# Performance work log

Measured on AMD Instinct MI355X. Metric: run time of the kernel, lower is better.

The kernel has to match this reference:

```python
import jax, jax.numpy as jnp
import numpy as np

EPS = 1e-5

def _bn_relu(y, mean, var, scale, bias):
    # y: (b, c, n); eval-mode batchnorm over channel axis, then ReLU
    inv = scale / jnp.sqrt(var + EPS)
    return jax.nn.relu((y - mean[None, :, None]) * inv[None, :, None] + bias[None, :, None])

def setup_inputs() -> dict:
    key = jax.random.key(0)
    ks = jax.random.split(key, 6)
    b, c, n, cr = 4, 256, 4096, 32
    inp = {
        'x': jax.random.normal(ks[0], (b, c, n), jnp.float32),
        'w_q': jax.random.normal(ks[1], (cr, c), jnp.float32) * (1.0 / np.sqrt(c)),
        'w_k': jax.random.normal(ks[2], (cr, c), jnp.float32) * (1.0 / np.sqrt(c)),
        'w_v': jax.random.normal(ks[3], (c, c), jnp.float32) * (1.0 / np.sqrt(c)),
        'bn1_scale': jnp.ones((cr,), jnp.float32), 'bn1_bias': jnp.zeros((cr,), jnp.float32),
        'bn1_mean': jnp.zeros((cr,), jnp.float32), 'bn1_var': jnp.ones((cr,), jnp.float32),
        'bn2_scale': jnp.ones((cr,), jnp.float32), 'bn2_bias': jnp.zeros((cr,), jnp.float32),
        'bn2_mean': jnp.zeros((cr,), jnp.float32), 'bn2_var': jnp.ones((cr,), jnp.float32),
        'bn3_scale': jnp.ones((c,), jnp.float32), 'bn3_bias': jnp.zeros((c,), jnp.float32),
        'bn3_mean': jnp.zeros((c,), jnp.float32), 'bn3_var': jnp.ones((c,), jnp.float32),
        'gamma': jax.random.normal(ks[4], (1,), jnp.float32),
    }
    return inp

def reference(x, w_q, w_k, w_v,
              bn1_scale, bn1_bias, bn1_mean, bn1_var,
              bn2_scale, bn2_bias, bn2_mean, bn2_var,
              bn3_scale, bn3_bias, bn3_mean, bn3_var,
              gamma):
    # x: (b, c, n). Original views as (b, c, n, 1) so width=1, height=n.
    b, c, n = x.shape
    # 1x1 conv == channel matmul, then BN+ReLU
    q = _bn_relu(jnp.einsum('oc,bcn->bon', w_q, x), bn1_mean, bn1_var, bn1_scale, bn1_bias)  # (b, c', n)
    k = _bn_relu(jnp.einsum('oc,bcn->bon', w_k, x), bn2_mean, bn2_var, bn2_scale, bn2_bias)  # (b, c', n)
    v = _bn_relu(jnp.einsum('oc,bcn->bon', w_v, x), bn3_mean, bn3_var, bn3_scale, bn3_bias)  # (b, c, n)
    # energy_H: (b, n, n) with -inf diagonal (self-attention along 'height')
    energy_h = jnp.einsum('bdi,bdj->bij', q, k)
    eye = jnp.eye(n, dtype=bool)
    energy_h = jnp.where(eye[None], -jnp.inf, energy_h)
    # energy_W: width=1 -> per-position self energy (b, n)
    energy_w = jnp.sum(q * k, axis=1)
    # softmax over concat of n H-logits and 1 W-logit
    att = jax.nn.softmax(jnp.concatenate([energy_h, energy_w[..., None]], axis=-1), axis=-1)  # (b, n, n+1)
    att_h = att[..., :n]        # (b, n, n), query i -> key j
    att_w = att[..., n]         # (b, n)
    out_h = jnp.einsum('bcj,bij->bci', v, att_h)   # aggregate values along height
    out_w = v * att_w[:, None, :]                  # width=1 self term
    out = gamma[0] * (out_h + out_w) + x
    return out
```

## Files before the change

kernel.cpp:

```cpp
#include <hip/hip_runtime.h>

#define Bb 4
#define Cc 256
#define Nn 4096
#define CR 32
#define EPS_BN 1e-5f
#define SHIFT2 28.853900817779268f
#define LOG2E  1.4426950408889634f
#define JSPLIT 4
#define JSL (Nn / JSPLIT)
#define TJ 64
#define NTILES (JSL / TJ)

typedef __attribute__((ext_vector_type(8))) short short8;
typedef __attribute__((ext_vector_type(4))) float f32x4;

__device__ inline unsigned int pk2(float a, float b) {
    __bf16 ha = (__bf16)a, hb = (__bf16)b;
    unsigned short ra = __builtin_bit_cast(unsigned short, ha);
    unsigned short rb = __builtin_bit_cast(unsigned short, hb);
    return ((unsigned int)rb << 16) | ra;
}
__device__ inline float blo(unsigned int u) { return __uint_as_float(u << 16); }
__device__ inline float bhi(unsigned int u) { return __uint_as_float(u & 0xffff0000u); }
__device__ inline float ex2(float x) { return __builtin_amdgcn_exp2f(x); }

__global__ __launch_bounds__(256) void qkv_kernel(
    const float* __restrict__ x,
    const float* __restrict__ wq, const float* __restrict__ wk, const float* __restrict__ wv,
    const float* __restrict__ bn1s, const float* __restrict__ bn1b, const float* __restrict__ bn1m, const float* __restrict__ bn1v,
    const float* __restrict__ bn2s, const float* __restrict__ bn2b, const float* __restrict__ bn2m, const float* __restrict__ bn2v,
    const float* __restrict__ bn3s, const float* __restrict__ bn3b, const float* __restrict__ bn3m, const float* __restrict__ bn3v,
    __bf16* __restrict__ Qt, __bf16* __restrict__ Kt, __bf16* __restrict__ Vb)
{
    __shared__ __align__(16) __bf16 F[16384];
    __shared__ __align__(16) float  sXf[4][32 * 40];
    __shared__ __align__(16) __bf16 sXt[4][2][32 * 40];

    const int tid = threadIdx.x;
    const int n0 = blockIdx.x * 128, g = blockIdx.y, b = blockIdx.z;
    const int lane = tid & 63, w = tid >> 6;
    const int l15 = lane & 15, l4 = lane >> 4;

    {
        int r = tid >> 2, q = tid & 3;
        int R = g * 64 + r;
        const float* src = (R < 32) ? (wq + (size_t)R * Cc)
                         : (R < 64) ? (wk + (size_t)(R - 32) * Cc)
                                    : (wv + (size_t)(R - 64) * Cc);
        int mt = r >> 4, l15r = r & 15;
#pragma unroll
        for (int u8 = 0; u8 < 8; ++u8) {
            float4 a = *(const float4*)&src[q * 64 + u8 * 8];
            float4 c2 = *(const float4*)&src[q * 64 + u8 * 8 + 4];
            uint4 p = { pk2(a.x,a.y), pk2(a.z,a.w), pk2(c2.x,c2.y), pk2(c2.z,c2.w) };
            int kc = 2 * q + (u8 >> 2), l4k = u8 & 3;
            *(uint4*)&F[(((kc * 4 + mt) * 64 + l4k * 16 + l15r)) * 8] = p;
        }
    }

    float*  sXfw  = &sXf[w][0];
    __bf16* sXtw0 = &sXt[w][0][0];
    __bf16* sXtw1 = &sXt[w][1][0];

    const int cr = lane >> 3, nq = lane & 7;
    const float* xbase = x + (size_t)(b * Cc + cr) * Nn + n0 + w * 32 + nq * 4;

    float4 xg[4];
#pragma unroll
    for (int it = 0; it < 4; ++it)
        xg[it] = *(const float4*)&xbase[(size_t)(it * 8) * Nn];

    __syncthreads();

    f32x4 acc[4][2];
#pragma unroll
    for (int mt = 0; mt < 4; ++mt)
#pragma unroll
        for (int nt = 0; nt < 2; ++nt) acc[mt][nt] = (f32x4){0.f, 0.f, 0.f, 0.f};

    for (int kc = 0; kc < 8; ++kc) {
#pragma unroll
        for (int it = 0; it < 4; ++it)
            *(float4*)&sXfw[(it * 8 + cr) * 40 + nq * 4] = xg[it];

        if (kc + 1 < 8) {
#pragma unroll
            for (int it = 0; it < 4; ++it)
                xg[it] = *(const float4*)&xbase[(size_t)((kc + 1) * 32 + it * 8) * Nn];
        }

#pragma unroll
        for (int s = 0; s < 2; ++s) {
            int n = lane & 31, c0 = (lane >> 5) * 8 + s * 16;
            float h[8], lo[8];
#pragma unroll
            for (int j = 0; j < 8; ++j) {
                float v = sXfw[(c0 + j) * 40 + n];
                float hh = (float)(__bf16)v;
                h[j] = hh; lo[j] = v - hh;
            }
            uint4 H = { pk2(h[0],h[1]), pk2(h[2],h[3]), pk2(h[4],h[5]), pk2(h[6],h[7]) };
            uint4 L = { pk2(lo[0],lo[1]), pk2(lo[2],lo[3]), pk2(lo[4],lo[5]), pk2(lo[6],lo[7]) };
            *(uint4*)&sXtw0[n * 40 + c0] = H;
            *(uint4*)&sXtw1[n * 40 + c0] = L;
        }

        short8 bh[2], bl[2];
#pragma unroll
        for (int nt = 0; nt < 2; ++nt) {
            bh[nt] = *(const short8*)&sXtw0[(nt * 16 + l15) * 40 + l4 * 8];
            bl[nt] = *(const short8*)&sXtw1[(nt * 16 + l15) * 40 + l4 * 8];
        }
#pragma unroll
        for (int mt = 0; mt < 4; ++mt) {
            short8 af = *(const short8*)&F[((kc * 4 + mt) * 64 + lane) * 8];
#pragma unroll
            for (int nt = 0; nt < 2; ++nt) {
                acc[mt][nt] = __builtin_amdgcn_mfma_f32_16x16x32_bf16(af, bh[nt], acc[mt][nt], 0, 0, 0);
                acc[mt][nt] = __builtin_amdgcn_mfma_f32_16x16x32_bf16(af, bl[nt], acc[mt][nt], 0, 0, 0);
            }
        }
    }

    if (g == 0) {
#pragma unroll
        for (int mt = 0; mt < 4; ++mt) {
            float scl[4], off[4];
#pragma unroll
            for (int r = 0; r < 4; ++r) {
                int R = mt * 16 + l4 * 4 + r;
                float s, o;
                if (R < 32) {
                    s = bn1s[R] * __frsqrt_rn(bn1v[R] + EPS_BN);
                    o = bn1b[R] - bn1m[R] * s;
                } else {
                    int row = R - 32;
                    s = bn2s[row] * __frsqrt_rn(bn2v[row] + EPS_BN);
                    o = bn2b[row] - bn2m[row] * s;
                    s *= LOG2E; o *= LOG2E;
                }
                scl[r] = s; off[r] = o;
            }
            __bf16* dst = (mt < 2) ? Qt : Kt;
            int d0 = (mt & 1) * 16 + l4 * 4;
#pragma unroll
            for (int nt = 0; nt < 2; ++nt) {
                f32x4 a = acc[mt][nt];
                float e0 = fmaxf(fmaf(a.x, scl[0], off[0]), 0.f);
                float e1 = fmaxf(fmaf(a.y, scl[1], off[1]), 0.f);
                float e2 = fmaxf(fmaf(a.z, scl[2], off[2]), 0.f);
                float e3 = fmaxf(fmaf(a.w, scl[3], off[3]), 0.f);
                uint2 p = { pk2(e0, e1), pk2(e2, e3) };
                int n = n0 + w * 32 + nt * 16 + l15;
                *(uint2*)&dst[(size_t)(b * Nn + n) * CR + d0] = p;
            }
        }
    } else {
        __bf16* oT = F;
        __syncthreads();
#pragma unroll
        for (int mt = 0; mt < 4; ++mt) {
            float scl[4], off[4];
#pragma unroll
            for (int r = 0; r < 4; ++r) {
                int row = (g - 1) * 64 + mt * 16 + l4 * 4 + r;
                float s = bn3s[row] * __frsqrt_rn(bn3v[row] + EPS_BN);
                scl[r] = s; off[r] = bn3b[row] - bn3m[row] * s;
            }
#pragma unroll
            for (int nt = 0; nt < 2; ++nt) {
                f32x4 a = acc[mt][nt];
                float e[4];
                e[0] = fmaxf(fmaf(a.x, scl[0], off[0]), 0.f);
                e[1] = fmaxf(fmaf(a.y, scl[1], off[1]), 0.f);
                e[2] = fmaxf(fmaf(a.z, scl[2], off[2]), 0.f);
                e[3] = fmaxf(fmaf(a.w, scl[3], off[3]), 0.f);
                int ncol = w * 32 + nt * 16 + l15;
#pragma unroll
                for (int r = 0; r < 4; ++r)
                    oT[(mt * 16 + l4 * 4 + r) * 136 + ncol] = (__bf16)e[r];
            }
        }
        __syncthreads();
        int rr = tid >> 2, qq = tid & 3;
        size_t vrow = (size_t)(b * Cc + (g - 1) * 64 + rr) * Nn + n0 + qq * 32;
#pragma unroll
        for (int e8 = 0; e8 < 4; ++e8)
            *(uint4*)&Vb[vrow + e8 * 8] = *(const uint4*)&oT[rr * 136 + qq * 32 + e8 * 8];
    }
}

__global__ __launch_bounds__(256) void attn_kernel(
    const __bf16* __restrict__ Qt, const __bf16* __restrict__ Kt,
    const __bf16* __restrict__ Vb,
    __bf16* __restrict__ PO, float* __restrict__ PL)
{
    __shared__ __align__(16) __bf16 sQ[64 * 40];
    __shared__ __align__(16) __bf16 sP[64 * 72];
    __shared__ __align__(16) float  sL[4][64];

    const int tid = threadIdx.x, lane = tid & 63, w = tid >> 6;
    const int b = blockIdx.z, js = blockIdx.y, iblk = blockIdx.x;
    const int i0 = iblk * 64;
    const int l15 = lane & 15, l4 = lane >> 4;

    {
        int i = tid >> 2, o = tid & 3;
        *(uint4*)&sQ[i * 40 + o * 8] =
            *(const uint4*)&Qt[(size_t)(b * Nn + i0 + i) * CR + o * 8];
    }
    __syncthreads();
    short8 qf[4];
#pragma unroll
    for (int it = 0; it < 4; ++it)
        qf[it] = *(const short8*)&sQ[(it * 16 + l15) * 40 + l4 * 8];

    f32x4 oacc[16];
#pragma unroll
    for (int z = 0; z < 16; ++z) oacc[z] = (f32x4){0.f, 0.f, 0.f, 0.f};
    float lp[4] = {0.f, 0.f, 0.f, 0.f};

    const size_t jb = (size_t)js * JSL;
    short8 kf = *(const short8*)&Kt[(size_t)(b * Nn + jb + 16 * w + l15) * CR + l4 * 8];

    for (int t = 0; t < NTILES; ++t) {
        const size_t j0 = jb + (size_t)t * TJ;

        short8 vf[8];
#pragma unroll
        for (int u = 0; u < 8; ++u) {
            int jh = u >> 2, ct = u & 3;
            int c = w * 64 + ct * 16 + l15;
            vf[u] = *(const short8*)&Vb[(size_t)(b * Cc + c) * Nn + j0 + (jh * 4 + l4) * 8];
        }

#pragma unroll
        for (int it = 0; it < 4; ++it) {
            f32x4 c0 = (f32x4){0.f, 0.f, 0.f, 0.f};
            c0 = __builtin_amdgcn_mfma_f32_16x16x32_bf16(kf, qf[it], c0, 0, 0, 0);
            float e0 = ex2(c0.x - SHIFT2);
            float e1 = ex2(c0.y - SHIFT2);
            float e2 = ex2(c0.z - SHIFT2);
            float e3 = ex2(c0.w - SHIFT2);
            lp[it] += (e0 + e1) + (e2 + e3);
            uint2 p2 = { pk2(e0, e1), pk2(e2, e3) };
            *(uint2*)&sP[(it * 16 + l15) * 72 + w * 16 + l4 * 4] = p2;
        }
        __syncthreads();

        if (t + 1 < NTILES)
            kf = *(const short8*)&Kt[(size_t)(b * Nn + j0 + TJ + 16 * w + l15) * CR + l4 * 8];

#pragma unroll
        for (int jh = 0; jh < 2; ++jh) {
            short8 pf[4];
#pragma unroll
            for (int it = 0; it < 4; ++it)
                pf[it] = *(const short8*)&sP[(it * 16 + l15) * 72 + jh * 32 + l4 * 8];
#pragma unroll
            for (int ct = 0; ct < 4; ++ct) {
#pragma unroll
                for (int it = 0; it < 4; ++it)
                    oacc[it * 4 + ct] = __builtin_amdgcn_mfma_f32_16x16x32_bf16(
                        pf[it], vf[jh * 4 + ct], oacc[it * 4 + ct], 0, 0, 0);
            }
        }
        __syncthreads();
    }

#pragma unroll
    for (int it = 0; it < 4; ++it) {
        float v = lp[it];
        v += __shfl_xor(v, 16);
        v += __shfl_xor(v, 32);
        if (lane < 16) sL[w][it * 16 + lane] = v;
    }
    __syncthreads();
    if (tid < 64)
        PL[(size_t)(js * Bb + b) * Nn + i0 + tid] =
            sL[0][tid] + sL[1][tid] + sL[2][tid] + sL[3][tid];

    const size_t base = (size_t)((js * Bb + b) * (Nn / 64) + iblk) * 16384;
#pragma unroll
    for (int it = 0; it < 4; ++it)
#pragma unroll
        for (int ct = 0; ct < 4; ++ct) {
            f32x4 a = oacc[it * 4 + ct];
            uint2 p = { pk2(a.x, a.y), pk2(a.z, a.w) };
            *(uint2*)&PO[base + (size_t)((((w * 4 + it) * 4 + ct) * 64 + lane)) * 4] = p;
        }
}

__global__ __launch_bounds__(256) void reduce_kernel(
    const __bf16* __restrict__ PO, const float* __restrict__ PL,
    const float* __restrict__ x, const float* __restrict__ gamma,
    float* __restrict__ out)
{
    __shared__ __align__(16) float oT[64 * 68];
    __shared__ float sLinv[64];

    const int tid = threadIdx.x;
    const int iblk = blockIdx.x, wq = blockIdx.y, b = blockIdx.z;
    const int i0 = iblk * 64;
    const int lane = tid & 63, ct = tid >> 6, l15 = lane & 15, l4 = lane >> 4;

    if (tid < 64) {
        float l = 0.f;
#pragma unroll
        for (int js = 0; js < JSPLIT; ++js)
            l += PL[(size_t)(js * Bb + b) * Nn + i0 + tid];
        sLinv[tid] = 1.0f / l;
    }

    float o[4][4];
#pragma unroll
    for (int it = 0; it < 4; ++it) {
        o[it][0] = o[it][1] = o[it][2] = o[it][3] = 0.f;
#pragma unroll
        for (int js = 0; js < JSPLIT; ++js) {
            size_t base = (size_t)((js * Bb + b) * (Nn / 64) + iblk) * 16384;
            uint2 v = *(const uint2*)&PO[base + (size_t)((((wq * 4 + it) * 4 + ct) * 64 + lane)) * 4];
            o[it][0] += blo(v.x); o[it][1] += bhi(v.x);
            o[it][2] += blo(v.y); o[it][3] += bhi(v.y);
        }
    }

    const int cl = ct * 16 + l15;
#pragma unroll
    for (int it = 0; it < 4; ++it) {
        float4 t4 = { o[it][0], o[it][1], o[it][2], o[it][3] };
        *(float4*)&oT[cl * 68 + it * 16 + l4 * 4] = t4;
    }
    __syncthreads();

    const float g = gamma[0];
    const int c_l = tid >> 2, icol = (tid & 3) * 16;
    const int cg = wq * 64 + c_l;
    const size_t gb = (size_t)(b * Cc + cg) * Nn + i0 + icol;
#pragma unroll
    for (int k4 = 0; k4 < 4; ++k4) {
        float4 ov = *(const float4*)&oT[c_l * 68 + icol + k4 * 4];
        float4 li = *(const float4*)&sLinv[icol + k4 * 4];
        float4 xv = *(const float4*)&x[gb + k4 * 4];
        float4 res;
        res.x = fmaf(g, ov.x * li.x, xv.x);
        res.y = fmaf(g, ov.y * li.y, xv.y);
        res.z = fmaf(g, ov.z * li.z, xv.z);
        res.w = fmaf(g, ov.w * li.w, xv.w);
        *(float4*)&out[gb + k4 * 4] = res;
    }
}

extern "C" void kernel_launch(void* const* d_in, const int* in_sizes, int n_in,
                              void* d_out, int out_size, void* d_ws, size_t ws_size,
                              hipStream_t stream)
{
    const float* x    = (const float*)d_in[0];
    const float* wq   = (const float*)d_in[1];
    const float* wk   = (const float*)d_in[2];
    const float* wv   = (const float*)d_in[3];
    const float* bn1s = (const float*)d_in[4];
    const float* bn1b = (const float*)d_in[5];
    const float* bn1m = (const float*)d_in[6];
    const float* bn1v = (const float*)d_in[7];
    const float* bn2s = (const float*)d_in[8];
    const float* bn2b = (const float*)d_in[9];
    const float* bn2m = (const float*)d_in[10];
    const float* bn2v = (const float*)d_in[11];
    const float* bn3s = (const float*)d_in[12];
    const float* bn3b = (const float*)d_in[13];
    const float* bn3m = (const float*)d_in[14];
    const float* bn3v = (const float*)d_in[15];
    const float* gmm  = (const float*)d_in[16];
    float* out = (float*)d_out;

    char* ws = (char*)d_ws;
    __bf16* Qt  = (__bf16*)(ws);
    __bf16* Kt  = (__bf16*)(ws + (1u << 20));
    __bf16* Vb  = (__bf16*)(ws + (2u << 20));
    char*   big = ws + (10u << 20);
    __bf16* PO  = (__bf16*)big;
    float*  PL  = (float*)(big + 33554432);

    qkv_kernel<<<dim3(Nn / 128, 5, Bb), 256, 0, stream>>>(
        x, wq, wk, wv,
        bn1s, bn1b, bn1m, bn1v,
        bn2s, bn2b, bn2m, bn2v,
        bn3s, bn3b, bn3m, bn3v,
        Qt, Kt, Vb);

    attn_kernel<<<dim3(Nn / 64, JSPLIT, Bb), 256, 0, stream>>>(Qt, Kt, Vb, PO, PL);

    reduce_kernel<<<dim3(Nn / 64, 4, Bb), 256, 0, stream>>>(PO, PL, x, gmm, out);
}
```

Before: 214.6 us.

## Give each wave a private 32x128 attention tile and drop block barriers

The attention kernel now splits the 64-query by 256-channel output so each wave owns 32 queries and 128 channels. Each wave computes its own P tile redundantly and stores it in wave-private, XOR-swizzled shared memory, which removes all __syncthreads in the inner loop and the shared staging of Q and the partial sums. V loads are split into two halves interleaved with the score computation. The trade-off is that the QK^T MFMAs and exponentials are duplicated across the two channel halves. The PO layout and the reduce kernel's indexing change to match.

```diff
diff --git a/kernel.cpp b/kernel.cpp
--- a/kernel.cpp
+++ b/kernel.cpp
@@ -196,99 +196,126 @@
     const __bf16* __restrict__ Vb,
     __bf16* __restrict__ PO, float* __restrict__ PL)
 {
-    __shared__ __align__(16) __bf16 sQ[64 * 40];
-    __shared__ __align__(16) __bf16 sP[64 * 72];
-    __shared__ __align__(16) float  sL[4][64];
+    __shared__ __align__(16) __bf16 sP[4][32 * 64];
 
     const int tid = threadIdx.x, lane = tid & 63, w = tid >> 6;
+    const int wi = w >> 1, wc = w & 1;
     const int b = blockIdx.z, js = blockIdx.y, iblk = blockIdx.x;
     const int i0 = iblk * 64;
-    const int l15 = lane & 15, l4 = lane >> 4;
-
-    {
-        int i = tid >> 2, o = tid & 3;
-        *(uint4*)&sQ[i * 40 + o * 8] =
-            *(const uint4*)&Qt[(size_t)(b * Nn + i0 + i) * CR + o * 8];
-    }
-    __syncthreads();
-    short8 qf[4];
-#pragma unroll
-    for (int it = 0; it < 4; ++it)
-        qf[it] = *(const short8*)&sQ[(it * 16 + l15) * 40 + l4 * 8];
-
-    f32x4 oacc[16];
-#pragma unroll
-    for (int z = 0; z < 16; ++z) oacc[z] = (f32x4){0.f, 0.f, 0.f, 0.f};
-    float lp[4] = {0.f, 0.f, 0.f, 0.f};
+    const int q = lane & 15, h = lane >> 4, q7 = lane & 7;
+
+    char* sPw = (char*)&sP[w][0];
+
+    short8 qf[2];
+#pragma unroll
+    for (int it = 0; it < 2; ++it)
+        qf[it] = *(const short8*)&Qt[(size_t)(b * Nn + i0 + wi * 32 + it * 16 + q) * CR + h * 8];
+
+    f32x4 oacc[2][8];
+#pragma unroll
+    for (int it = 0; it < 2; ++it)
+#pragma unroll
+        for (int ct = 0; ct < 8; ++ct) oacc[it][ct] = (f32x4){0.f, 0.f, 0.f, 0.f};
+    float lp[2] = {0.f, 0.f};
 
     const size_t jb = (size_t)js * JSL;
-    short8 kf = *(const short8*)&Kt[(size_t)(b * Nn + jb + 16 * w + l15) * CR + l4 * 8];
+
+    short8 kf[4];
+#pragma unroll
+    for (int s = 0; s < 4; ++s)
+        kf[s] = *(const short8*)&Kt[(size_t)(b * Nn + jb + s * 16 + q) * CR + h * 8];
+
+    const __bf16* vbase = Vb + (size_t)(b * Cc + wc * 128 + q) * Nn;
 
     for (int t = 0; t < NTILES; ++t) {
         const size_t j0 = jb + (size_t)t * TJ;
 
         short8 vf[8];
 #pragma unroll
-        for (int u = 0; u < 8; ++u) {
-            int jh = u >> 2, ct = u & 3;
-            int c = w * 64 + ct * 16 + l15;
-            vf[u] = *(const short8*)&Vb[(size_t)(b * Cc + c) * Nn + j0 + (jh * 4 + l4) * 8];
-        }
-
-#pragma unroll
-        for (int it = 0; it < 4; ++it) {
-            f32x4 c0 = (f32x4){0.f, 0.f, 0.f, 0.f};
-            c0 = __builtin_amdgcn_mfma_f32_16x16x32_bf16(kf, qf[it], c0, 0, 0, 0);
-            float e0 = ex2(c0.x - SHIFT2);
-            float e1 = ex2(c0.y - SHIFT2);
-            float e2 = ex2(c0.z - SHIFT2);
-            float e3 = ex2(c0.w - SHIFT2);
-            lp[it] += (e0 + e1) + (e2 + e3);
-            uint2 p2 = { pk2(e0, e1), pk2(e2, e3) };
-            *(uint2*)&sP[(it * 16 + l15) * 72 + w * 16 + l4 * 4] = p2;
-        }
-        __syncthreads();
-
-        if (t + 1 < NTILES)
-            kf = *(const short8*)&Kt[(size_t)(b * Nn + j0 + TJ + 16 * w + l15) * CR + l4 * 8];
-
-#pragma unroll
-        for (int jh = 0; jh < 2; ++jh) {
-            short8 pf[4];
-#pragma unroll
-            for (int it = 0; it < 4; ++it)
-                pf[it] = *(const short8*)&sP[(it * 16 + l15) * 72 + jh * 32 + l4 * 8];
-#pragma unroll
-            for (int ct = 0; ct < 4; ++ct) {
-#pragma unroll
-                for (int it = 0; it < 4; ++it)
-                    oacc[it * 4 + ct] = __builtin_amdgcn_mfma_f32_16x16x32_bf16(
-                        pf[it], vf[jh * 4 + ct], oacc[it * 4 + ct], 0, 0, 0);
-            }
-        }
-        __syncthreads();
-    }
-
-#pragma unroll
-    for (int it = 0; it < 4; ++it) {
+        for (int ct = 0; ct < 8; ++ct)
+            vf[ct] = *(const short8*)&vbase[(size_t)(ct * 16) * Nn + j0 + h * 8];
+
+#pragma unroll
+        for (int jss = 0; jss < 2; ++jss) {
+#pragma unroll
+            for (int it = 0; it < 2; ++it) {
+                f32x4 c0 = (f32x4){0.f, 0.f, 0.f, 0.f};
+                c0 = __builtin_amdgcn_mfma_f32_16x16x32_bf16(kf[jss], qf[it], c0, 0, 0, 0);
+                float e0 = ex2(c0.x - SHIFT2), e1 = ex2(c0.y - SHIFT2);
+                float e2 = ex2(c0.z - SHIFT2), e3 = ex2(c0.w - SHIFT2);
+                lp[it] += (e0 + e1) + (e2 + e3);
+                uint2 p2 = { pk2(e0, e1), pk2(e2, e3) };
+                *(uint2*)(sPw + ((it * 16 + q) << 7) + ((((jss << 1) + (h >> 1)) ^ q7) << 4) + ((h & 1) << 3)) = p2;
+            }
+        }
+
+        {
+            short8 pa[2];
+#pragma unroll
+            for (int it = 0; it < 2; ++it)
+                pa[it] = *(const short8*)(sPw + ((it * 16 + q) << 7) + ((h ^ q7) << 4));
+#pragma unroll
+            for (int ct = 0; ct < 8; ++ct) {
+                oacc[0][ct] = __builtin_amdgcn_mfma_f32_16x16x32_bf16(pa[0], vf[ct], oacc[0][ct], 0, 0, 0);
+                oacc[1][ct] = __builtin_amdgcn_mfma_f32_16x16x32_bf16(pa[1], vf[ct], oacc[1][ct], 0, 0, 0);
+            }
+        }
+
+#pragma unroll
+        for (int ct = 0; ct < 8; ++ct)
+            vf[ct] = *(const short8*)&vbase[(size_t)(ct * 16) * Nn + j0 + 32 + h * 8];
+
+#pragma unroll
+        for (int jss = 2; jss < 4; ++jss) {
+#pragma unroll
+            for (int it = 0; it < 2; ++it) {
+                f32x4 c0 = (f32x4){0.f, 0.f, 0.f, 0.f};
+                c0 = __builtin_amdgcn_mfma_f32_16x16x32_bf16(kf[jss], qf[it], c0, 0, 0, 0);
+                float e0 = ex2(c0.x - SHIFT2), e1 = ex2(c0.y - SHIFT2);
+                float e2 = ex2(c0.z - SHIFT2), e3 = ex2(c0.w - SHIFT2);
+                lp[it] += (e0 + e1) + (e2 + e3);
+                uint2 p2 = { pk2(e0, e1), pk2(e2, e3) };
+                *(uint2*)(sPw + ((it * 16 + q) << 7) + ((((jss << 1) + (h >> 1)) ^ q7) << 4) + ((h & 1) << 3)) = p2;
+            }
+        }
+
+        if (t + 1 < NTILES) {
+#pragma unroll
+            for (int s = 0; s < 4; ++s)
+                kf[s] = *(const short8*)&Kt[(size_t)(b * Nn + j0 + TJ + s * 16 + q) * CR + h * 8];
+        }
+
+        {
+            short8 pa[2];
+#pragma unroll
+            for (int it = 0; it < 2; ++it)
+                pa[it] = *(const short8*)(sPw + ((it * 16 + q) << 7) + (((4 + h) ^ q7) << 4));
+#pragma unroll
+            for (int ct = 0; ct < 8; ++ct) {
+                oacc[0][ct] = __builtin_amdgcn_mfma_f32_16x16x32_bf16(pa[0], vf[ct], oacc[0][ct], 0, 0, 0);
+                oacc[1][ct] = __builtin_amdgcn_mfma_f32_16x16x32_bf16(pa[1], vf[ct], oacc[1][ct], 0, 0, 0);
+            }
+        }
+    }
+
+#pragma unroll
+    for (int it = 0; it < 2; ++it) {
         float v = lp[it];
         v += __shfl_xor(v, 16);
         v += __shfl_xor(v, 32);
-        if (lane < 16) sL[w][it * 16 + lane] = v;
-    }
-    __syncthreads();
-    if (tid < 64)
-        PL[(size_t)(js * Bb + b) * Nn + i0 + tid] =
-            sL[0][tid] + sL[1][tid] + sL[2][tid] + sL[3][tid];
+        if (wc == 0 && lane < 16)
+            PL[(size_t)(js * Bb + b) * Nn + i0 + wi * 32 + it * 16 + lane] = v;
+    }
 
     const size_t base = (size_t)((js * Bb + b) * (Nn / 64) + iblk) * 16384;
 #pragma unroll
-    for (int it = 0; it < 4; ++it)
-#pragma unroll
-        for (int ct = 0; ct < 4; ++ct) {
-            f32x4 a = oacc[it * 4 + ct];
+    for (int it = 0; it < 2; ++it)
+#pragma unroll
+        for (int ct = 0; ct < 8; ++ct) {
+            f32x4 a = oacc[it][ct];
             uint2 p = { pk2(a.x, a.y), pk2(a.z, a.w) };
-            *(uint2*)&PO[base + (size_t)((((w * 4 + it) * 4 + ct) * 64 + lane)) * 4] = p;
+            int gi = wi * 2 + it, gc = wc * 8 + ct;
+            *(uint2*)&PO[base + (size_t)((gi * 16 + gc) * 64 + lane) * 4] = p;
         }
 }
 
@@ -320,7 +347,7 @@
 #pragma unroll
         for (int js = 0; js < JSPLIT; ++js) {
             size_t base = (size_t)((js * Bb + b) * (Nn / 64) + iblk) * 16384;
-            uint2 v = *(const uint2*)&PO[base + (size_t)((((wq * 4 + it) * 4 + ct) * 64 + lane)) * 4];
+            uint2 v = *(const uint2*)&PO[base + (size_t)((it * 16 + wq * 4 + ct) * 64 + lane) * 4];
             o[it][0] += blo(v.x); o[it][1] += bhi(v.x);
             o[it][2] += blo(v.y); o[it][3] += bhi(v.y);
         }
```

Result: slower. 275.8 us (+28.5%).
